# Optimization experiments

Hardware: AMD Instinct MI355X
Metric: run time of the kernel (lower is better)

## Reference

```python
import jax, jax.numpy as jnp
import numpy as np

_BN_EPS = 1e-5


def _conv2d(x, w, b, dilation):
    # x: (B,C,T,F), w: (O,I,k,k); 'same' padding per DilatedConv: (k-1)*d//2
    k = w.shape[-1]
    pad = (k - 1) * dilation // 2
    y = jax.lax.conv_general_dilated(
        x, w, window_strides=(1, 1),
        padding=[(pad, pad), (pad, pad)],
        rhs_dilation=(dilation, dilation),
        dimension_numbers=('NCHW', 'OIHW', 'NCHW'))
    return y + b[None, :, None, None]


def _gate(x, w, b, gamma, beta, mean, var, dilation):
    # conv -> BatchNorm2d (inference) -> chunk -> tanh * sigmoid
    y = _conv2d(x, w, b, dilation)
    scale = gamma * jax.lax.rsqrt(var + _BN_EPS)
    y = (y - mean[None, :, None, None]) * scale[None, :, None, None] + beta[None, :, None, None]
    a, g = jnp.split(y, 2, axis=1)
    return jnp.tanh(a) * jax.nn.sigmoid(g)


def _gru(x, wih, whh, bih, bhh):
    # forward-direction GRU (PyTorch gate order r,z,n). x: (T,N,I) -> (T,N,H)
    H = whh.shape[-1]
    gi = jnp.einsum('tni,hi->tnh', x, wih) + bih  # (T,N,3H), input projections

    def step(h, gi_t):
        gh = h @ whh.T + bhh
        r = jax.nn.sigmoid(gi_t[:, :H] + gh[:, :H])
        z = jax.nn.sigmoid(gi_t[:, H:2 * H] + gh[:, H:2 * H])
        n = jnp.tanh(gi_t[:, 2 * H:] + r * gh[:, 2 * H:])
        h_new = (1.0 - z) * n + z * h
        return h_new, h_new

    h0 = jnp.zeros((x.shape[1], H), x.dtype)
    _, ys = jax.lax.scan(step, h0, gi)
    return ys


def setup_inputs() -> dict:
    key = jax.random.key(0)
    ks = jax.random.split(key, 32)
    B, T, F, C, G = 8, 512, 256, 16, 8
    Cg = C // G  # 2
    d = {'x': jax.random.normal(ks[0], (B, 2, T, F), jnp.float32)}
    ki = 1
    for name, cin in zip(('g1', 'g2', 'g3', 'g4'), (2, C, C, C)):
        d[name + '_w'] = jax.random.normal(ks[ki], (2 * C, cin, 3, 3), jnp.float32) * (0.5 / np.sqrt(cin * 9.0)); ki += 1
        d[name + '_b'] = jax.random.normal(ks[ki], (2 * C,), jnp.float32) * 0.05; ki += 1
        d[name + '_gamma'] = 1.0 + 0.1 * jax.random.normal(ks[ki], (2 * C,), jnp.float32); ki += 1
        d[name + '_beta'] = 0.1 * jax.random.normal(ks[ki], (2 * C,), jnp.float32); ki += 1
        d[name + '_mean'] = jnp.zeros((2 * C,), jnp.float32)
        d[name + '_var'] = jnp.ones((2 * C,), jnp.float32)
    d['gru_wih'] = jax.random.normal(ks[ki], (G, 3 * Cg, Cg), jnp.float32) * 0.3; ki += 1
    d['gru_whh'] = jax.random.normal(ks[ki], (G, 3 * Cg, Cg), jnp.float32) * 0.3; ki += 1
    d['gru_bih'] = jax.random.normal(ks[ki], (G, 3 * Cg), jnp.float32) * 0.1; ki += 1
    d['gru_bhh'] = jax.random.normal(ks[ki], (G, 3 * Cg), jnp.float32) * 0.1; ki += 1
    d['out_w'] = jax.random.normal(ks[ki], (1, C), jnp.float32) * 0.3; ki += 1
    d['out_b'] = jax.random.normal(ks[ki], (1,), jnp.float32) * 0.05
    return d


def reference(x, g1_w, g1_b, g1_gamma, g1_beta, g1_mean, g1_var,
              g2_w, g2_b, g2_gamma, g2_beta, g2_mean, g2_var,
              g3_w, g3_b, g3_gamma, g3_beta, g3_mean, g3_var,
              g4_w, g4_b, g4_gamma, g4_beta, g4_mean, g4_var,
              gru_wih, gru_whh, gru_bih, gru_bhh, out_w, out_b):
    out = _gate(x, g1_w, g1_b, g1_gamma, g1_beta, g1_mean, g1_var, 1)
    out = _gate(out, g2_w, g2_b, g2_gamma, g2_beta, g2_mean, g2_var, 2)
    out = _gate(out, g3_w, g3_b, g3_gamma, g3_beta, g3_mean, g3_var, 4)
    out = _gate(out, g4_w, g4_b, g4_gamma, g4_beta, g4_mean, g4_var, 8)
    B, C, T, F = out.shape
    G = gru_wih.shape[0]
    Cg = C // G
    # split channels into G groups of Cg, run GRU over time, batched over (B*F)
    xg = out.reshape(B, G, Cg, T, F).transpose(1, 3, 0, 4, 2).reshape(G, T, B * F, Cg)
    ys = jax.vmap(_gru)(xg, gru_wih, gru_whh, gru_bih, gru_bhh)  # (G,T,B*F,Cg)
    merged = ys.reshape(G, T, B, F, Cg).transpose(2, 0, 4, 1, 3).reshape(B, C, T, F)
    # 1x1 out_conv -> 1 channel
    return jnp.einsum('bctf,oc->botf', merged, out_w) + out_b[None, :, None, None]
```

## Files before the change

kernel.cpp:

```cpp
#include <hip/hip_runtime.h>

#define Bb 8
#define Tt 512
#define Ff 256
#define Cc 16
#define TF (Tt*Ff)
#define TROW 528
#define FROW 272
#define CELL 32
#define WROWB (144*CELL)
#define BUFBYTES ((size_t)Bb*TROW*FROW*CELL)

typedef _Float16 half8 __attribute__((ext_vector_type(8)));
typedef __attribute__((ext_vector_type(4))) float f32x4;

typedef const __attribute__((address_space(1))) void* gas1_t;
typedef __attribute__((address_space(3))) void* las3_t;
#define GLOAD_LDS(g, l) __builtin_amdgcn_global_load_lds((gas1_t)(const void*)(g), (las3_t)(void*)(l), 16, 0, 0)

#define WAIT_VM32 0x8F70
#define WAIT_VM48 0xCF70

__device__ __forceinline__ float fexp2(float x) { return __builtin_amdgcn_exp2f(x); }

__device__ __forceinline__ float fast_sigmoid(float x) {
    return __builtin_amdgcn_rcpf(1.0f + fexp2(-1.4426950408889634f * x));
}
__device__ __forceinline__ float fast_tanh(float x) {
    return 1.0f - 2.0f * __builtin_amdgcn_rcpf(fexp2(2.8853900817779268f * x) + 1.0f);
}

__device__ __forceinline__ unsigned short hbits(float x) {
    _Float16 h = (_Float16)x;
    return __builtin_bit_cast(unsigned short, h);
}
__device__ __forceinline__ float h2f(unsigned short u) {
    return (float)__builtin_bit_cast(_Float16, u);
}
__device__ __forceinline__ f32x4 mfma_f16(half8 a, half8 b, f32x4 c) {
    return __builtin_amdgcn_mfma_f32_16x16x32_f16(a, b, c, 0, 0, 0);
}

__device__ __forceinline__ float2 f2fma(float2 a, float s, float2 c) {
    return make_float2(fmaf(a.x, s, c.x), fmaf(a.y, s, c.y));
}
__device__ __forceinline__ float2 sig2(float2 u) {
    float e0 = fexp2(-u.x), e1 = fexp2(-u.y);
    return make_float2(__builtin_amdgcn_rcpf(1.f + e0), __builtin_amdgcn_rcpf(1.f + e1));
}
__device__ __forceinline__ float2 tanh2(float2 u) {
    float e0 = fexp2(u.x + u.x), e1 = fexp2(u.y + u.y);
    return make_float2(1.f - 2.f * __builtin_amdgcn_rcpf(e0 + 1.f),
                       1.f - 2.f * __builtin_amdgcn_rcpf(e1 + 1.f));
}

__global__ __launch_bounds__(256)
void setup_all(const float* __restrict__ x1, const float* __restrict__ w1, const float* __restrict__ b1,
               const float* __restrict__ gm1, const float* __restrict__ bt1,
               const float* __restrict__ mn1, const float* __restrict__ vr1,
               const float* __restrict__ w2, const float* __restrict__ b2, const float* __restrict__ gm2,
               const float* __restrict__ bt2, const float* __restrict__ mn2, const float* __restrict__ vr2,
               const float* __restrict__ w3, const float* __restrict__ b3, const float* __restrict__ gm3,
               const float* __restrict__ bt3, const float* __restrict__ mn3, const float* __restrict__ vr3,
               const float* __restrict__ w4, const float* __restrict__ b4, const float* __restrict__ gm4,
               const float* __restrict__ bt4, const float* __restrict__ mn4, const float* __restrict__ vr4,
               char* __restrict__ bufA, char* __restrict__ bufB,
               char* __restrict__ wpreAll, float* __restrict__ bpreAll)
{
    const int blk = blockIdx.x;
    const int tid = threadIdx.x;
    if (blk < 3) {
        const float *w, *bias, *gamma, *beta, *mean, *var;
        if (blk == 0)      { w = w2; bias = b2; gamma = gm2; beta = bt2; mean = mn2; var = vr2; }
        else if (blk == 1) { w = w3; bias = b3; gamma = gm3; beta = bt3; mean = mn3; var = vr3; }
        else               { w = w4; bias = b4; gamma = gm4; beta = bt4; mean = mn4; var = vr4; }
        char* wpre = wpreAll + blk * 20480;
        float* bpre = bpreAll + blk * 32;
        if (tid < 32) {
            float s = gamma[tid] * rsqrtf(var[tid] + 1e-5f);
            bpre[tid] = (bias[tid] - mean[tid]) * s + beta[tid];
        }
        for (int i = tid; i < 4608; i += 256) {
            int co = i / 144, r = i - co * 144;
            int ci = r / 9, tap = r - ci * 9;
            float s = gamma[co] * rsqrtf(var[co] + 1e-5f);
            float wv = w[(co * 16 + ci) * 9 + tap] * s;
            unsigned short hi = hbits(wv);
            unsigned short lo = hbits((wv - h2f(hi)) * 2048.0f);
            int ks = tap >> 1, tp = tap & 1;
            int kl = tp * 16 + ci;
            int qq = kl >> 3, jj = kl & 7;
            int sub = qq ^ (co & 3);
            *(unsigned short*)(wpre + ((0 * 5 + ks) * 32 + co) * 64 + sub * 16 + jj * 2) = hi;
            *(unsigned short*)(wpre + ((1 * 5 + ks) * 32 + co) * 64 + sub * 16 + jj * 2) = lo;
        }
        for (int i = tid; i < 1024; i += 256) {
            int p = i >> 9, rem = i & 511;
            int co = rem >> 4, kl = 16 + (rem & 15);
            int qq = kl >> 3, jj = kl & 7;
            int sub = qq ^ (co & 3);
            *(unsigned short*)(wpre + ((p * 5 + 4) * 32 + co) * 64 + sub * 16 + jj * 2) = 0;
        }
    } else if (blk < 787) {
        int idx = (blk - 3) * 256 + tid;
        int which = idx >= 100352;
        int r0 = which ? idx - 100352 : idx;
        int b = r0 / 12544, c = r0 - b * 12544;
        int tp, fp;
        if (c < 4352) { int row = c / 272; fp = c - row * 272; tp = row < 8 ? row : 512 + row; }
        else { int c2 = c - 4352; tp = 8 + (c2 >> 4); int fi = c2 & 15; fp = fi < 8 ? fi : 256 + fi; }
        char* base = (which ? bufB : bufA) + ((size_t)(b * TROW + tp) * FROW + fp) * CELL;
        float4 z = make_float4(0.f, 0.f, 0.f, 0.f);
        float4* p = (float4*)base;
        p[0] = z; p[1] = z;
    } else {
        __shared__ float xs[2][6][66];
        __shared__ float wl[18 * 32];
        __shared__ float bnsL[32], bnoL[32];
        int bb = blk - 787;
        int fx = bb & 3;
        int ty = (bb >> 2) & 127;
        int b  = bb >> 9;
        const int f0 = fx * 64;
        const int t0 = ty * 4;
        const int fl = tid & 63;
        const int tr = (tid >> 6) & 1;
        const int h  = tid >> 7;

        if (tid < 32) {
            float s = gm1[tid] * rsqrtf(vr1[tid] + 1e-5f);
            bnsL[tid] = s;
            bnoL[tid] = (b1[tid] - mn1[tid]) * s + bt1[tid];
        }
        for (int i = tid; i < 576; i += 256) {
            int co = i & 31, rest = i >> 5;
            int ci = rest / 9, tap = rest - ci * 9;
            wl[rest * 32 + co] = w1[(co * 2 + ci) * 9 + tap];
        }
        for (int i = tid; i < 792; i += 256) {
            int ci = i / 396, r = i - ci * 396;
            int row = r / 66, col = r - row * 66;
            int t_in = t0 + row - 1, f_in = f0 + col - 1;
            float v = 0.f;
            if (t_in >= 0 && t_in < Tt && f_in >= 0 && f_in < Ff)
                v = x1[((size_t)(b * 2 + ci) * Tt + t_in) * Ff + f_in];
            xs[ci][row][col] = v;
        }
        __syncthreads();

        float acc[2][16];
        #pragma unroll
        for (int q = 0; q < 2; q++)
            #pragma unroll
            for (int j = 0; j < 16; j++) acc[q][j] = 0.f;

        #pragma unroll
        for (int ci = 0; ci < 2; ci++) {
            float win[4][3];
            #pragma unroll
            for (int r = 0; r < 4; r++)
                #pragma unroll
                for (int c = 0; c < 3; c++)
                    win[r][c] = xs[ci][2 * tr + r][fl + c];
            #pragma unroll
            for (int dt = 0; dt < 3; dt++)
                #pragma unroll
                for (int kf = 0; kf < 3; kf++) {
                    float xv0 = win[dt][kf];
                    float xv1 = win[dt + 1][kf];
                    const float* wrow = wl + (ci * 9 + dt * 3 + kf) * 32 + h * 8;
                    float wv[16];
                    *(float4*)(wv)      = *(const float4*)(wrow);
                    *(float4*)(wv + 4)  = *(const float4*)(wrow + 4);
                    *(float4*)(wv + 8)  = *(const float4*)(wrow + 16);
                    *(float4*)(wv + 12) = *(const float4*)(wrow + 20);
                    #pragma unroll
                    for (int j = 0; j < 16; j++) {
                        acc[0][j] = fmaf(xv0, wv[j], acc[0][j]);
                        acc[1][j] = fmaf(xv1, wv[j], acc[1][j]);
                    }
                }
        }

        #pragma unroll
        for (int q = 0; q < 2; q++) {
            int t = t0 + 2 * tr + q;
            int fp = f0 + fl + 8;
            int sw = fp & 1;
            char* cell = bufA + ((size_t)(b * TROW + t + 8) * FROW + fp) * CELL;
            unsigned short hv[8];
            #pragma unroll
            for (int j = 0; j < 8; j++) {
                int ca = h * 8 + j, cg = 16 + h * 8 + j;
                float av = acc[q][j]     * bnsL[ca] + bnoL[ca];
                float gv = acc[q][8 + j] * bnsL[cg] + bnoL[cg];
                hv[j] = hbits(fast_tanh(av) * fast_sigmoid(gv));
            }
            uint4 P;
            P.x = (unsigned)hv[0] | ((unsigned)hv[1] << 16);
            P.y = (unsigned)hv[2] | ((unsigned)hv[3] << 16);
            P.z = (unsigned)hv[4] | ((unsigned)hv[5] << 16);
            P.w = (unsigned)hv[6] | ((unsigned)hv[7] << 16);
            *(uint4*)(cell + ((h ^ sw) * 16)) = P;
        }
    }
}

template<int DIL, int WRITE_F32>
__global__ __launch_bounds__(256, 2)
void gate_mfma(const char* __restrict__ actIn, const char* __restrict__ wpre,
               const float* __restrict__ bpre, char* __restrict__ outBuf)
{
    __shared__ char actL[32768];
    const int tg = blockIdx.x, fh = blockIdx.y, b = blockIdx.z;
    const int tid = threadIdx.x;
    const int w = tid >> 6, lane = tid & 63;
    const int n = lane & 15, q = lane >> 4;
    const int tsel = w >> 1, fsel = w & 1;
    constexpr int GPC = 128 / DIL;
    const int rcl = tg / GPC, m = tg - rcl * GPC;
    const int t0 = rcl + 4 * m * DIL;
    const int f0 = fh * 128;

    half8 aH[5][2], aL[5][2];
    #pragma unroll
    for (int ks = 0; ks < 5; ks++)
        #pragma unroll
        for (int ct = 0; ct < 2; ct++) {
            int co = ct * 16 + n;
            int sub = q ^ (co & 3);
            aH[ks][ct] = *(const half8*)(wpre + (size_t)((0 * 5 + ks) * 32 + co) * 64 + sub * 16);
            aL[ks][ct] = *(const half8*)(wpre + (size_t)((5 + ks) * 32 + co) * 64 + sub * 16);
        }

    #pragma unroll
    for (int i = 0; i < 6; i++) {
        int tp = t0 + 8 + (i - 1) * DIL;
        const char* src = actIn + ((size_t)(b * TROW + tp) * FROW + f0) * CELL;
        char* dst = actL + i * WROWB;
        GLOAD_LDS(src + tid * 16, dst + tid * 16);
        if (tid < 64)
            GLOAD_LDS(src + (224 + tid) * 16, dst + (224 + tid) * 16);
    }
    __syncthreads();

    const int fbl = fsel * 64;
    f32x4 accH[2][4][2] = {}, accL[2][4][2] = {};

    #pragma unroll
    for (int ks = 0; ks < 5; ks++) {
        const int tapA = 2 * ks;
        const int tapB = (2 * ks + 1 > 8) ? 8 : 2 * ks + 1;
        const int rowA = tapA / 3, dfA = (tapA % 3 - 1) * DIL;
        const int rowB = tapB / 3, dfB = (tapB % 3 - 1) * DIL;
        int tapSel = q >> 1;
        int rowt = tapSel ? rowB : rowA;
        int df  = tapSel ? dfB : dfA;
        int cih = q & 1;
        #pragma unroll
        for (int tj = 0; tj < 2; tj++) {
            const int jj = 2 * tsel + tj;
            const char* rbase = actL + (jj + rowt) * WROWB;
            #pragma unroll
            for (int nt = 0; nt < 4; nt++) {
                int fp = 8 + fbl + nt * 16 + n + df;
                const char* cell = rbase + fp * CELL;
                half8 bF = *(const half8*)(cell + ((cih ^ (fp & 1)) * 16));
                #pragma unroll
                for (int ct = 0; ct < 2; ct++) {
                    accH[tj][nt][ct] = mfma_f16(aH[ks][ct], bF, accH[tj][nt][ct]);
                    accL[tj][nt][ct] = mfma_f16(aL[ks][ct], bF, accL[tj][nt][ct]);
                }
            }
        }
    }

    float4 bA = *(const float4*)(bpre + q * 4);
    float4 bG = *(const float4*)(bpre + 16 + q * 4);
    const float CL = 4.8828125e-4f;
    __syncthreads();

    if (WRITE_F32) {
        float* Ef = (float*)actL;
        #pragma unroll
        for (int tj = 0; tj < 2; tj++) {
            const int jj = 2 * tsel + tj;
            #pragma unroll
            for (int nt = 0; nt < 4; nt++) {
                float a0 = accH[tj][nt][0].x + CL * accL[tj][nt][0].x + bA.x;
                float a1 = accH[tj][nt][0].y + CL * accL[tj][nt][0].y + bA.y;
                float a2 = accH[tj][nt][0].z + CL * accL[tj][nt][0].z + bA.z;
                float a3 = accH[tj][nt][0].w + CL * accL[tj][nt][0].w + bA.w;
                float g0 = accH[tj][nt][1].x + CL * accL[tj][nt][1].x + bG.x;
                float g1 = accH[tj][nt][1].y + CL * accL[tj][nt][1].y + bG.y;
                float g2 = accH[tj][nt][1].z + CL * accL[tj][nt][1].z + bG.z;
                float g3 = accH[tj][nt][1].w + CL * accL[tj][nt][1].w + bG.w;
                float r[4];
                r[0] = fast_tanh(a0) * fast_sigmoid(g0);
                r[1] = fast_tanh(a1) * fast_sigmoid(g1);
                r[2] = fast_tanh(a2) * fast_sigmoid(g2);
                r[3] = fast_tanh(a3) * fast_sigmoid(g3);
                int fl = fbl + nt * 16 + n;
                #pragma unroll
                for (int j = 0; j < 4; j++)
                    Ef[(jj * 16 + q * 4 + j) * 128 + fl] = r[j];
            }
        }
        __syncthreads();
        float* gp = (float*)outBuf;
        #pragma unroll
        for (int k = 0; k < 8; k++) {
            int linear = k * 256 + tid;
            int jj2 = linear >> 9;
            int rem = linear & 511;
            int c = rem >> 5, fq = rem & 31;
            int tt = t0 + jj2 * DIL;
            *(float4*)(gp + (size_t)(b * 16 + c) * TF + tt * Ff + fh * 128 + fq * 4) =
                *(const float4*)(Ef + (jj2 * 16 + c) * 128 + fq * 4);
        }
    } else {
        char* Eo = actL;
        #pragma unroll
        for (int tj = 0; tj < 2; tj++) {
            const int jj = 2 * tsel + tj;
            #pragma unroll
            for (int nt = 0; nt < 4; nt++) {
                float a0 = accH[tj][nt][0].x + CL * accL[tj][nt][0].x + bA.x;
                float a1 = accH[tj][nt][0].y + CL * accL[tj][nt][0].y + bA.y;
                float a2 = accH[tj][nt][0].z + CL * accL[tj][nt][0].z + bA.z;
                float a3 = accH[tj][nt][0].w + CL * accL[tj][nt][0].w + bA.w;
                float g0 = accH[tj][nt][1].x + CL * accL[tj][nt][1].x + bG.x;
                float g1 = accH[tj][nt][1].y + CL * accL[tj][nt][1].y + bG.y;
                float g2 = accH[tj][nt][1].z + CL * accL[tj][nt][1].z + bG.z;
                float g3 = accH[tj][nt][1].w + CL * accL[tj][nt][1].w + bG.w;
                unsigned short hv[4];
                hv[0] = hbits(fast_tanh(a0) * fast_sigmoid(g0));
                hv[1] = hbits(fast_tanh(a1) * fast_sigmoid(g1));
                hv[2] = hbits(fast_tanh(a2) * fast_sigmoid(g2));
                hv[3] = hbits(fast_tanh(a3) * fast_sigmoid(g3));
                int fl = fbl + nt * 16 + n;
                int sw = (fh * 128 + fl + 8) & 1;
                uint2 pk;
                pk.x = (unsigned)hv[0] | ((unsigned)hv[1] << 16);
                pk.y = (unsigned)hv[2] | ((unsigned)hv[3] << 16);
                char* base = Eo + (jj * 128 + fl) * CELL;
                *(uint2*)(base + ((q >> 1) ^ sw) * 16 + (q & 1) * 8) = pk;
            }
        }
        __syncthreads();
        #pragma unroll
        for (int k = 0; k < 4; k++) {
            int linear = k * 256 + tid;
            int jj2 = linear >> 8;
            int idx = linear & 255;
            int tt = t0 + jj2 * DIL;
            char* dstRow = outBuf + ((size_t)(b * TROW + tt + 8) * FROW + fh * 128 + 8) * CELL;
            *(uint4*)(dstRow + idx * 16) = *(const uint4*)(Eo + jj2 * 4096 + idx * 16);
        }
    }
}

__global__ __launch_bounds__(64)
void gru_kernel(const float* __restrict__ xin, const float* __restrict__ wih,
                const float* __restrict__ whh, const float* __restrict__ bih,
                const float* __restrict__ bhh, const float* __restrict__ out_w,
                float* __restrict__ part)
{
    __shared__ float ldsF[3 * 4096];
    const int lane = threadIdx.x;
    const int fsl = blockIdx.x & 3;
    const int g = (blockIdx.x >> 2) & 7;
    const int b = blockIdx.x >> 5;

    const float L2E = 1.4426950408889634f;
    float2 WiX[3], WiY[3], WhX[3], WhY[3], Bi[3], Bh[3];
    #pragma unroll
    for (int p = 0; p < 3; p++) {
        WiX[p] = make_float2(wih[g * 12 + (2 * p) * 2 + 0] * L2E, wih[g * 12 + (2 * p + 1) * 2 + 0] * L2E);
        WiY[p] = make_float2(wih[g * 12 + (2 * p) * 2 + 1] * L2E, wih[g * 12 + (2 * p + 1) * 2 + 1] * L2E);
        WhX[p] = make_float2(whh[g * 12 + (2 * p) * 2 + 0] * L2E, whh[g * 12 + (2 * p + 1) * 2 + 0] * L2E);
        WhY[p] = make_float2(whh[g * 12 + (2 * p) * 2 + 1] * L2E, whh[g * 12 + (2 * p + 1) * 2 + 1] * L2E);
        Bi[p] = make_float2(bih[g * 6 + 2 * p] * L2E, bih[g * 6 + 2 * p + 1] * L2E);
        Bh[p] = make_float2(bhh[g * 6 + 2 * p] * L2E, bhh[g * 6 + 2 * p + 1] * L2E);
    }
    const float ow0 = out_w[2 * g], ow1 = out_w[2 * g + 1];

    const int sub = lane & 15, cch = (lane >> 4) & 1, tpr = lane >> 5;
    const float* gsrc = xin + ((size_t)(b * Cc + 2 * g + cch) * Tt + tpr) * Ff + fsl * 64 + sub * 4;

    float* poBase = part + ((size_t)((b * 8 + g) * 4 + fsl)) * 32768;

    #define STAGE(bsel, chunk)                                                \
    {                                                                         \
        char* ldst = (char*)(ldsF + (bsel) * 4096);                           \
        const float* gs = gsrc + (size_t)(chunk) * 32 * Ff;                   \
        _Pragma("unroll")                                                     \
        for (int j = 0; j < 16; j++)                                          \
            GLOAD_LDS(gs + 2 * j * Ff, ldst + j * 1024);                      \
    }

    float2 hP = make_float2(0.f, 0.f);
    STAGE(0, 0); STAGE(1, 1); STAGE(2, 2);

    for (int k = 0; k < 16; k++) {
        if (k) {
            int cs = k + 2; if (cs >= 16) cs -= 16;
            int bs = k + 2; bs -= (bs / 3) * 3;
            STAGE(bs, cs);
            __builtin_amdgcn_sched_barrier(0);
            __builtin_amdgcn_s_waitcnt(WAIT_VM48);
            __builtin_amdgcn_sched_barrier(0);
        } else {
            __builtin_amdgcn_sched_barrier(0);
            __builtin_amdgcn_s_waitcnt(WAIT_VM32);
            __builtin_amdgcn_sched_barrier(0);
        }
        int bc = k - (k / 3) * 3;
        const float* cbase = ldsF + bc * 4096;
        float2 outR[16];
        #pragma unroll
        for (int tt = 0; tt < 32; tt++) {
            const float* cell = cbase + (tt >> 1) * 256 + (tt & 1) * 128;
            float x0 = cell[lane];
            float x1 = cell[64 + lane];
            float2 giR = f2fma(WiY[0], x1, f2fma(WiX[0], x0, Bi[0]));
            float2 giZ = f2fma(WiY[1], x1, f2fma(WiX[1], x0, Bi[1]));
            float2 giN = f2fma(WiY[2], x1, f2fma(WiX[2], x0, Bi[2]));
            float2 ghR = f2fma(WhY[0], hP.y, f2fma(WhX[0], hP.x, Bh[0]));
            float2 ghZ = f2fma(WhY[1], hP.y, f2fma(WhX[1], hP.x, Bh[1]));
            float2 ghN = f2fma(WhY[2], hP.y, f2fma(WhX[2], hP.x, Bh[2]));
            float2 rP = sig2(make_float2(giR.x + ghR.x, giR.y + ghR.y));
            float2 zP = sig2(make_float2(giZ.x + ghZ.x, giZ.y + ghZ.y));
            float2 nP = tanh2(make_float2(fmaf(rP.x, ghN.x, giN.x), fmaf(rP.y, ghN.y, giN.y)));
            hP = make_float2(fmaf(zP.x, hP.x - nP.x, nP.x), fmaf(zP.y, hP.y - nP.y, nP.y));
            float o = fmaf(hP.x, ow0, hP.y * ow1);
            if (tt & 1) outR[tt >> 1].y = o; else outR[tt >> 1].x = o;
        }
        #pragma unroll
        for (int j = 0; j < 16; j++)
            *(float2*)(poBase + (k * 16 + j) * 128 + lane * 2) = outR[j];
    }
    #undef STAGE
}

__global__ __launch_bounds__(256)
void out_kernel(const float* __restrict__ part, const float* __restrict__ out_b,
                float* __restrict__ out)
{
    int idx = blockIdx.x * 256 + threadIdx.x;
    int f = idx & 255;
    int tp = (idx >> 8) & 255;
    int b = idx >> 16;
    int fsl = f >> 6, ln = f & 63;
    const float* base = part + ((size_t)(b * 8) * 4 + fsl) * 32768 + tp * 128 + ln * 2;
    float ob = out_b[0];
    float s0 = ob, s1 = ob;
    #pragma unroll
    for (int g = 0; g < 8; g++) {
        float2 v = *(const float2*)(base + (size_t)g * 131072);
        s0 += v.x; s1 += v.y;
    }
    float* op = out + ((size_t)b * Tt + 2 * tp) * Ff + f;
    op[0] = s0;
    op[Ff] = s1;
}

extern "C" void kernel_launch(void* const* d_in, const int* in_sizes, int n_in,
                              void* d_out, int out_size, void* d_ws, size_t ws_size,
                              hipStream_t stream) {
    char* bufA = (char*)d_ws;
    char* bufB = bufA + BUFBYTES;
    float* gruF = (float*)(bufB + BUFBYTES);
    char* wpre = (char*)gruF + (size_t)Bb * Cc * TF * 4;
    float* bpre = (float*)(wpre + 3 * 20480);

    setup_all<<<787 + 4096, 256, 0, stream>>>(
        (const float*)d_in[0],
        (const float*)d_in[1],  (const float*)d_in[2],  (const float*)d_in[3],
        (const float*)d_in[4],  (const float*)d_in[5],  (const float*)d_in[6],
        (const float*)d_in[7],  (const float*)d_in[8],  (const float*)d_in[9],
        (const float*)d_in[10], (const float*)d_in[11], (const float*)d_in[12],
        (const float*)d_in[13], (const float*)d_in[14], (const float*)d_in[15],
        (const float*)d_in[16], (const float*)d_in[17], (const float*)d_in[18],
        (const float*)d_in[19], (const float*)d_in[20], (const float*)d_in[21],
        (const float*)d_in[22], (const float*)d_in[23], (const float*)d_in[24],
        bufA, bufB, wpre, bpre);

    dim3 grid(128, 2, Bb), blk(256);
    gate_mfma<2, 0><<<grid, blk, 0, stream>>>(bufA, wpre,         bpre,      bufB);
    gate_mfma<4, 0><<<grid, blk, 0, stream>>>(bufB, wpre + 20480, bpre + 32, bufA);
    gate_mfma<8, 1><<<grid, blk, 0, stream>>>(bufA, wpre + 40960, bpre + 64, (char*)gruF);

    gru_kernel<<<Bb * 8 * 4, 64, 0, stream>>>(
        gruF, (const float*)d_in[25], (const float*)d_in[26], (const float*)d_in[27],
        (const float*)d_in[28], (const float*)d_in[29], (float*)bufA);

    out_kernel<<<2048, 256, 0, stream>>>(
        (const float*)bufA, (const float*)d_in[30], (float*)d_out);
}
```

Before: 302.9 us.

## Split GRU hidden units across lanes with DPP exchange and two waves per block

The GRU kernel now gives each hidden unit its own lane and exchanges the partner unit's state with a DPP row shuffle, instead of one lane computing both units. Each wave covers 32 frequency bins, so there are twice as many wavefronts (256 blocks of 128 threads) working on the serial recurrence. This shortens the per-lane dependency chain and raises parallelism. Staging moves to double buffering issued after compute with adjusted waitcnts, and the partial-output layout and out_kernel reduction change to sum the two unit halves.

```diff
diff --git a/kernel.cpp b/kernel.cpp
--- a/kernel.cpp
+++ b/kernel.cpp
@@ -18,8 +18,9 @@
 typedef __attribute__((address_space(3))) void* las3_t;
 #define GLOAD_LDS(g, l) __builtin_amdgcn_global_load_lds((gas1_t)(const void*)(g), (las3_t)(void*)(l), 16, 0, 0)
 
-#define WAIT_VM32 0x8F70
-#define WAIT_VM48 0xCF70
+#define WAIT_VM8  0x0F78
+#define WAIT_VM24 0x4F78
+#define WAIT_VM40 0x8F78
 
 __device__ __forceinline__ float fexp2(float x) { return __builtin_amdgcn_exp2f(x); }
 
@@ -40,18 +41,10 @@
 __device__ __forceinline__ f32x4 mfma_f16(half8 a, half8 b, f32x4 c) {
     return __builtin_amdgcn_mfma_f32_16x16x32_f16(a, b, c, 0, 0, 0);
 }
-
-__device__ __forceinline__ float2 f2fma(float2 a, float s, float2 c) {
-    return make_float2(fmaf(a.x, s, c.x), fmaf(a.y, s, c.y));
-}
-__device__ __forceinline__ float2 sig2(float2 u) {
-    float e0 = fexp2(-u.x), e1 = fexp2(-u.y);
-    return make_float2(__builtin_amdgcn_rcpf(1.f + e0), __builtin_amdgcn_rcpf(1.f + e1));
-}
-__device__ __forceinline__ float2 tanh2(float2 u) {
-    float e0 = fexp2(u.x + u.x), e1 = fexp2(u.y + u.y);
-    return make_float2(1.f - 2.f * __builtin_amdgcn_rcpf(e0 + 1.f),
-                       1.f - 2.f * __builtin_amdgcn_rcpf(e1 + 1.f));
+__device__ __forceinline__ float dpp_swap8(float x) {
+    int xi = __builtin_bit_cast(int, x);
+    int r = __builtin_amdgcn_mov_dpp(xi, 0x128, 0xf, 0xf, true);
+    return __builtin_bit_cast(float, r);
 }
 
 __global__ __launch_bounds__(256)
@@ -360,85 +353,91 @@
     }
 }
 
-__global__ __launch_bounds__(64)
+__global__ __launch_bounds__(128)
 void gru_kernel(const float* __restrict__ xin, const float* __restrict__ wih,
                 const float* __restrict__ whh, const float* __restrict__ bih,
                 const float* __restrict__ bhh, const float* __restrict__ out_w,
                 float* __restrict__ part)
 {
-    __shared__ float ldsF[3 * 4096];
-    const int lane = threadIdx.x;
-    const int fsl = blockIdx.x & 3;
+    __shared__ float ldsF[2][3 * 2048];
+    const int tid = threadIdx.x;
+    const int wv = tid >> 6, lane = tid & 63;
+    const int b = blockIdx.x >> 5;
     const int g = (blockIdx.x >> 2) & 7;
-    const int b = blockIdx.x >> 5;
+    const int fblk = (blockIdx.x & 3) * 2 + wv;
+    const int f0 = fblk * 32;
+
+    const int row = lane >> 4;
+    const int u = (lane >> 3) & 1;
+    const int fi = (lane & 7) | (row << 3);
 
     const float L2E = 1.4426950408889634f;
-    float2 WiX[3], WiY[3], WhX[3], WhY[3], Bi[3], Bh[3];
+    float Wi0[3], Wi1[3], Whs[3], Who[3], Bi[3], Bh[3];
     #pragma unroll
     for (int p = 0; p < 3; p++) {
-        WiX[p] = make_float2(wih[g * 12 + (2 * p) * 2 + 0] * L2E, wih[g * 12 + (2 * p + 1) * 2 + 0] * L2E);
-        WiY[p] = make_float2(wih[g * 12 + (2 * p) * 2 + 1] * L2E, wih[g * 12 + (2 * p + 1) * 2 + 1] * L2E);
-        WhX[p] = make_float2(whh[g * 12 + (2 * p) * 2 + 0] * L2E, whh[g * 12 + (2 * p + 1) * 2 + 0] * L2E);
-        WhY[p] = make_float2(whh[g * 12 + (2 * p) * 2 + 1] * L2E, whh[g * 12 + (2 * p + 1) * 2 + 1] * L2E);
-        Bi[p] = make_float2(bih[g * 6 + 2 * p] * L2E, bih[g * 6 + 2 * p + 1] * L2E);
-        Bh[p] = make_float2(bhh[g * 6 + 2 * p] * L2E, bhh[g * 6 + 2 * p + 1] * L2E);
-    }
-    const float ow0 = out_w[2 * g], ow1 = out_w[2 * g + 1];
-
-    const int sub = lane & 15, cch = (lane >> 4) & 1, tpr = lane >> 5;
-    const float* gsrc = xin + ((size_t)(b * Cc + 2 * g + cch) * Tt + tpr) * Ff + fsl * 64 + sub * 4;
-
-    float* poBase = part + ((size_t)((b * 8 + g) * 4 + fsl)) * 32768;
-
-    #define STAGE(bsel, chunk)                                                \
-    {                                                                         \
-        char* ldst = (char*)(ldsF + (bsel) * 4096);                           \
-        const float* gs = gsrc + (size_t)(chunk) * 32 * Ff;                   \
-        _Pragma("unroll")                                                     \
-        for (int j = 0; j < 16; j++)                                          \
-            GLOAD_LDS(gs + 2 * j * Ff, ldst + j * 1024);                      \
-    }
-
-    float2 hP = make_float2(0.f, 0.f);
-    STAGE(0, 0); STAGE(1, 1); STAGE(2, 2);
+        int rw = p * 2 + u;
+        Wi0[p] = wih[g * 12 + rw * 2 + 0] * L2E;
+        Wi1[p] = wih[g * 12 + rw * 2 + 1] * L2E;
+        Whs[p] = whh[g * 12 + rw * 2 + u] * L2E;
+        Who[p] = whh[g * 12 + rw * 2 + (1 - u)] * L2E;
+        Bi[p]  = bih[g * 6 + rw] * L2E;
+        Bh[p]  = bhh[g * 6 + rw] * L2E;
+    }
+    const float ow = out_w[2 * g + u];
+
+    const int s = lane & 7, cch = (lane >> 3) & 1, trr = lane >> 4;
+    const float* gsrc = xin + ((size_t)(b * Cc + 2 * g + cch) * Tt + trr) * Ff + f0 + s * 4;
+    float* ldsW = ldsF[wv];
+
+    float* poW = part + ((((size_t)(b * 8 + g) * 8 + fblk) * 256) * 128) + u * 64 + fi * 2;
+
+    #define STAGE(bsel, chunk)                                                 \
+    {                                                                          \
+        char* ldst = (char*)(ldsW + (bsel) * 2048) + lane * 16;                \
+        const float* gs = gsrc + (size_t)(chunk) * 32 * Ff;                    \
+        _Pragma("unroll")                                                      \
+        for (int i = 0; i < 8; i++)                                            \
+            GLOAD_LDS(gs + i * 4 * Ff, ldst + i * 1024);                       \
+    }
+
+    float h = 0.f;
+    STAGE(0, 0); STAGE(1, 1);
 
     for (int k = 0; k < 16; k++) {
-        if (k) {
-            int cs = k + 2; if (cs >= 16) cs -= 16;
-            int bs = k + 2; bs -= (bs / 3) * 3;
-            STAGE(bs, cs);
-            __builtin_amdgcn_sched_barrier(0);
-            __builtin_amdgcn_s_waitcnt(WAIT_VM48);
-            __builtin_amdgcn_sched_barrier(0);
-        } else {
-            __builtin_amdgcn_sched_barrier(0);
-            __builtin_amdgcn_s_waitcnt(WAIT_VM32);
-            __builtin_amdgcn_sched_barrier(0);
-        }
+        __builtin_amdgcn_sched_barrier(0);
+        if (k == 0)      __builtin_amdgcn_s_waitcnt(WAIT_VM8);
+        else if (k == 1) __builtin_amdgcn_s_waitcnt(WAIT_VM24);
+        else             __builtin_amdgcn_s_waitcnt(WAIT_VM40);
+        __builtin_amdgcn_sched_barrier(0);
         int bc = k - (k / 3) * 3;
-        const float* cbase = ldsF + bc * 4096;
+        const float* cbase = ldsW + bc * 2048;
         float2 outR[16];
         #pragma unroll
         for (int tt = 0; tt < 32; tt++) {
-            const float* cell = cbase + (tt >> 1) * 256 + (tt & 1) * 128;
-            float x0 = cell[lane];
-            float x1 = cell[64 + lane];
-            float2 giR = f2fma(WiY[0], x1, f2fma(WiX[0], x0, Bi[0]));
-            float2 giZ = f2fma(WiY[1], x1, f2fma(WiX[1], x0, Bi[1]));
-            float2 giN = f2fma(WiY[2], x1, f2fma(WiX[2], x0, Bi[2]));
-            float2 ghR = f2fma(WhY[0], hP.y, f2fma(WhX[0], hP.x, Bh[0]));
-            float2 ghZ = f2fma(WhY[1], hP.y, f2fma(WhX[1], hP.x, Bh[1]));
-            float2 ghN = f2fma(WhY[2], hP.y, f2fma(WhX[2], hP.x, Bh[2]));
-            float2 rP = sig2(make_float2(giR.x + ghR.x, giR.y + ghR.y));
-            float2 zP = sig2(make_float2(giZ.x + ghZ.x, giZ.y + ghZ.y));
-            float2 nP = tanh2(make_float2(fmaf(rP.x, ghN.x, giN.x), fmaf(rP.y, ghN.y, giN.y)));
-            hP = make_float2(fmaf(zP.x, hP.x - nP.x, nP.x), fmaf(zP.y, hP.y - nP.y, nP.y));
-            float o = fmaf(hP.x, ow0, hP.y * ow1);
+            const float* cell = cbase + (tt >> 2) * 256 + (tt & 3) * 64;
+            float x0 = cell[fi];
+            float x1 = cell[32 + fi];
+            float ho = dpp_swap8(h);
+            float gir = fmaf(Wi1[0], x1, fmaf(Wi0[0], x0, Bi[0]));
+            float giz = fmaf(Wi1[1], x1, fmaf(Wi0[1], x0, Bi[1]));
+            float gin = fmaf(Wi1[2], x1, fmaf(Wi0[2], x0, Bi[2]));
+            float ghr = fmaf(Who[0], ho, fmaf(Whs[0], h, Bh[0]));
+            float ghz = fmaf(Who[1], ho, fmaf(Whs[1], h, Bh[1]));
+            float ghn = fmaf(Who[2], ho, fmaf(Whs[2], h, Bh[2]));
+            float r = __builtin_amdgcn_rcpf(1.f + fexp2(-(gir + ghr)));
+            float z = __builtin_amdgcn_rcpf(1.f + fexp2(-(giz + ghz)));
+            float an = fmaf(r, ghn, gin);
+            float nv = fmaf(-2.f, __builtin_amdgcn_rcpf(fexp2(an + an) + 1.f), 1.f);
+            h = fmaf(z, h - nv, nv);
+            float o = h * ow;
             if (tt & 1) outR[tt >> 1].y = o; else outR[tt >> 1].x = o;
         }
+        int cs = k + 2; cs &= 15;
+        int bs = k + 2; bs -= (bs / 3) * 3;
+        STAGE(bs, cs);
         #pragma unroll
         for (int j = 0; j < 16; j++)
-            *(float2*)(poBase + (k * 16 + j) * 128 + lane * 2) = outR[j];
+            *(float2*)(poW + (k * 16 + j) * 128) = outR[j];
     }
     #undef STAGE
 }
@@ -451,15 +450,17 @@
     int f = idx & 255;
     int tp = (idx >> 8) & 255;
     int b = idx >> 16;
-    int fsl = f >> 6, ln = f & 63;
-    const float* base = part + ((size_t)(b * 8) * 4 + fsl) * 32768 + tp * 128 + ln * 2;
+    int fsl = f >> 5, fi = f & 31;
+    const float* base = part + (size_t)b * 2097152 + (size_t)fsl * 32768 + tp * 128 + fi * 2;
     float ob = out_b[0];
     float s0 = ob, s1 = ob;
     #pragma unroll
-    for (int g = 0; g < 8; g++) {
-        float2 v = *(const float2*)(base + (size_t)g * 131072);
-        s0 += v.x; s1 += v.y;
-    }
+    for (int g = 0; g < 8; g++)
+        #pragma unroll
+        for (int u = 0; u < 2; u++) {
+            float2 v = *(const float2*)(base + (size_t)g * 262144 + u * 64);
+            s0 += v.x; s1 += v.y;
+        }
     float* op = out + ((size_t)b * Tt + 2 * tp) * Ff + f;
     op[0] = s0;
     op[Ff] = s1;
@@ -473,6 +474,7 @@
     float* gruF = (float*)(bufB + BUFBYTES);
     char* wpre = (char*)gruF + (size_t)Bb * Cc * TF * 4;
     float* bpre = (float*)(wpre + 3 * 20480);
+    float* partF = (float*)bufA;
 
     setup_all<<<787 + 4096, 256, 0, stream>>>(
         (const float*)d_in[0],
@@ -491,10 +493,10 @@
     gate_mfma<4, 0><<<grid, blk, 0, stream>>>(bufB, wpre + 20480, bpre + 32, bufA);
     gate_mfma<8, 1><<<grid, blk, 0, stream>>>(bufA, wpre + 40960, bpre + 64, (char*)gruF);
 
-    gru_kernel<<<Bb * 8 * 4, 64, 0, stream>>>(
+    gru_kernel<<<256, 128, 0, stream>>>(
         gruF, (const float*)d_in[25], (const float*)d_in[26], (const float*)d_in[27],
-        (const float*)d_in[28], (const float*)d_in[29], (float*)bufA);
+        (const float*)d_in[28], (const float*)d_in[29], partF);
 
     out_kernel<<<2048, 256, 0, stream>>>(
-        (const float*)bufA, (const float*)d_in[30], (float*)d_out);
-}
+        partF, (const float*)d_in[30], (float*)d_out);
+}
```

Result: faster. 273.6 us (-9.7%).
